# Optimization experiments

Hardware: AMD Instinct MI355X
Metric: run time of the kernel (lower is better)

## Reference

```python
import jax, jax.numpy as jnp
import numpy as np

# Config mirrors module init: C=12 channels, include_time=True -> d=13, depth=3
# sig_channels = d + d^2 + d^3 = 2379

def setup_inputs() -> dict:
    key = jax.random.key(0)
    k1, k2, k3 = jax.random.split(key, 3)
    N, C, J, T, L = 8, 12, 25, 64, 5
    d = C + 1
    sig_channels = d + d * d + d ** 3  # 2379
    out_dim = 256
    x = jax.random.normal(k1, (N, C, J, T, L), dtype=jnp.float32)
    W = jax.random.normal(k2, (out_dim, sig_channels), dtype=jnp.float32) / np.sqrt(sig_channels)
    b = jax.random.normal(k3, (out_dim,), dtype=jnp.float32) * 0.01
    return {"x": x, "W": W, "b": b}


def _signature_depth3(path):
    """Truncated (depth 3) path signature with zero basepoint.
    path: [B, L, d] -> sig: [B, d + d^2 + d^3]
    Chen's identity: s <- s * exp(dx), with exp(dx)_n = dx^{(x)n} / n!
    """
    B, L, d = path.shape
    # basepoint=True: prepend zeros, then take increments
    inc = jnp.diff(jnp.concatenate([jnp.zeros((B, 1, d), path.dtype), path], axis=1), axis=1)  # [B, L, d]

    def step(carry, dx):
        s1, s2, s3 = carry  # [B,d], [B,d*d], [B,d^3]
        e2 = 0.5 * jnp.einsum('bi,bj->bij', dx, dx)                     # [B,d,d]
        e3 = (jnp.einsum('bij,bk->bijk', e2, dx) / 3.0).reshape(B, d ** 3)  # dx^3/6
        n1 = s1 + dx
        n2 = s2 + jnp.einsum('bi,bj->bij', s1, dx).reshape(B, d * d) + e2.reshape(B, d * d)
        n3 = (s3
              + jnp.einsum('bij,bk->bijk', s2.reshape(B, d, d), dx).reshape(B, d ** 3)
              + jnp.einsum('bi,bjk->bijk', s1, e2).reshape(B, d ** 3)
              + e3)
        return (n1, n2, n3), None

    init = (jnp.zeros((B, d), path.dtype),
            jnp.zeros((B, d * d), path.dtype),
            jnp.zeros((B, d ** 3), path.dtype))
    (s1, s2, s3), _ = jax.lax.scan(step, init, jnp.moveaxis(inc, 1, 0))
    return jnp.concatenate([s1, s2, s3], axis=-1)


def reference(x, W, b):
    N, C, J, T, L = x.shape
    B = J * T * N
    # windowed gather: block (i*T+j)*N..(..+1)*N = x[:,:,i,j,:].permute(0,2,1)
    path = jnp.transpose(x, (2, 3, 0, 4, 1)).reshape(B, L, C)  # [J*T*N, L, C]
    # Augment include_time=True: append time channel linspace(0,1,L)
    t = jnp.linspace(0.0, 1.0, L, dtype=path.dtype)
    path = jnp.concatenate([path, jnp.broadcast_to(t[None, :, None], (B, L, 1))], axis=-1)
    sig = _signature_depth3(path)                 # [B, 2379]
    z = sig @ W.T + b                             # [B, out_dim]
    # scatter back: res[:, :, i, j] = z[(i*T+j)*N : ...]
    return jnp.transpose(z.reshape(J, T, N, -1), (2, 3, 0, 1))  # [N, out_dim, J, T]
```

## Files before the change

### kernel.cpp

```cpp
#include <hip/hip_runtime.h>
#include <hip/hip_bf16.h>

typedef float f32x4 __attribute__((ext_vector_type(4)));
typedef short s16x8 __attribute__((ext_vector_type(8)));

#define SIGC 2379
#define KPAD 2432
#define NKT  76
#define NKT_HALF 38
#define SROW 2440
#define NPATH 12800


__device__ inline void split2(float v, __hip_bfloat16* h, __hip_bfloat16* l) {
    __hip_bfloat16 hh = __float2bfloat16(v);
    *h = hh;
    *l = __float2bfloat16(v - __bfloat162float(hh));
}

__device__ inline void gload_lds16(const __hip_bfloat16* g, __hip_bfloat16* l) {
    __builtin_amdgcn_global_load_lds(
        (const __attribute__((address_space(1))) void*)g,
        (__attribute__((address_space(3))) void*)l,
        16, 0, 0);
}

__global__ __launch_bounds__(256) void wconv_kernel(const float* __restrict__ W,
                                                    __hip_bfloat16* __restrict__ Wh,
                                                    __hip_bfloat16* __restrict__ Wl)
{
    int k = blockIdx.x * 256 + threadIdx.x;
    int n = blockIdx.y;
    if (k >= KPAD) return;
    float v = (k < SIGC) ? W[(size_t)n * SIGC + k] : 0.0f;
    size_t off = ((size_t)(n >> 4) * NKT + (k >> 5)) * 512 + ((k >> 3) & 3) * 128 + (n & 15) * 8 + (k & 7);
    split2(v, &Wh[off], &Wl[off]);
}

__global__ __launch_bounds__(256) void sig_kernel(const float* __restrict__ x,
                                                  __hip_bfloat16* __restrict__ Ah,
                                                  __hip_bfloat16* __restrict__ Al_,
                                                  int r_start)
{
    __shared__ float inc_s[4][5][16];
    __shared__ __align__(16) __hip_bfloat16 hi_s[4][SROW];
    __shared__ __align__(16) __hip_bfloat16 lo_s[4][SROW];

    const int t = threadIdx.x;
    const int w = t >> 6;
    const int lane = t & 63;

    const int p0 = lane;
    const int p1 = lane + 64;
    const int p2 = lane + 128;
    const bool has2 = (p2 < 169);
    const int i0 = p0 / 13, j0 = p0 - i0 * 13;
    const int i1 = p1 / 13, j1 = p1 - i1 * 13;
    const int i2 = p2 / 13, j2 = p2 - i2 * 13;

    for (int pp = 0; pp < 4; ++pp) {
        const int r = r_start + blockIdx.x * 16 + pp * 4 + w;
        const int nn = r & 7;
        const int jj = (r >> 3) & 63;
        const int ii = r >> 9;

        __syncthreads();
        if (lane < 13) {
            if (lane < 12) {
                const float* px = x + ((size_t)(nn * 12 + lane) * 1600 + ii * 64 + jj) * 5;
                float prev = 0.0f;
                #pragma unroll
                for (int l = 0; l < 5; ++l) {
                    float v = px[l];
                    inc_s[w][l][lane] = v - prev;
                    prev = v;
                }
            } else {
                inc_s[w][0][12] = 0.0f;
                #pragma unroll
                for (int l = 1; l < 5; ++l) inc_s[w][l][12] = 0.25f;
            }
        }
        __syncthreads();

        float s1i0 = 0.0f, s1i1 = 0.0f, s1i2 = 0.0f;
        float s2p0 = 0.0f, s2p1 = 0.0f, s2p2 = 0.0f;
        float s1own = 0.0f;
        float s3a[13], s3b[13], s3c[13];
        #pragma unroll
        for (int k = 0; k < 13; ++k) { s3a[k] = 0.0f; s3b[k] = 0.0f; s3c[k] = 0.0f; }

        for (int l = 0; l < 5; ++l) {
            float dxl[13];
            #pragma unroll
            for (int k = 0; k < 13; ++k) dxl[k] = inc_s[w][l][k];

            {
                float dxi = inc_s[w][l][i0];
                float dxj = inc_s[w][l][j0];
                float C   = s2p0 + 0.5f * dxj * (s1i0 + dxi * (1.0f / 3.0f));
                #pragma unroll
                for (int k = 0; k < 13; ++k) s3a[k] += dxl[k] * C;
                s2p0 += s1i0 * dxj + 0.5f * dxi * dxj;
                s1i0 += dxi;
            }
            {
                float dxi = inc_s[w][l][i1];
                float dxj = inc_s[w][l][j1];
                float C   = s2p1 + 0.5f * dxj * (s1i1 + dxi * (1.0f / 3.0f));
                #pragma unroll
                for (int k = 0; k < 13; ++k) s3b[k] += dxl[k] * C;
                s2p1 += s1i1 * dxj + 0.5f * dxi * dxj;
                s1i1 += dxi;
            }
            if (has2) {
                float dxi = inc_s[w][l][i2];
                float dxj = inc_s[w][l][j2];
                float C   = s2p2 + 0.5f * dxj * (s1i2 + dxi * (1.0f / 3.0f));
                #pragma unroll
                for (int k = 0; k < 13; ++k) s3c[k] += dxl[k] * C;
                s2p2 += s1i2 * dxj + 0.5f * dxi * dxj;
                s1i2 += dxi;
            }
            if (lane < 13) s1own += inc_s[w][l][lane];
        }

        if (lane < 13) split2(s1own, &hi_s[w][lane], &lo_s[w][lane]);
        split2(s2p0, &hi_s[w][13 + p0], &lo_s[w][13 + p0]);
        split2(s2p1, &hi_s[w][13 + p1], &lo_s[w][13 + p1]);
        if (has2) split2(s2p2, &hi_s[w][13 + p2], &lo_s[w][13 + p2]);
        #pragma unroll
        for (int k = 0; k < 13; ++k) split2(s3a[k], &hi_s[w][182 + p0 * 13 + k], &lo_s[w][182 + p0 * 13 + k]);
        #pragma unroll
        for (int k = 0; k < 13; ++k) split2(s3b[k], &hi_s[w][182 + p1 * 13 + k], &lo_s[w][182 + p1 * 13 + k]);
        if (has2) {
            #pragma unroll
            for (int k = 0; k < 13; ++k) split2(s3c[k], &hi_s[w][182 + p2 * 13 + k], &lo_s[w][182 + p2 * 13 + k]);
        }
        if (lane < KPAD - SIGC) {
            hi_s[w][SIGC + lane] = __float2bfloat16(0.0f);
            lo_s[w][SIGC + lane] = __float2bfloat16(0.0f);
        }

        __syncthreads();

        const int rtl = blockIdx.x;
        const int rr = t & 3, ks = (t >> 2) & 3, ts = t >> 4;
        #pragma unroll
        for (int it2 = 0; it2 < 5; ++it2) {
            int kt = it2 * 16 + ts;
            if (kt < NKT) {
                size_t off = ((size_t)rtl * NKT + kt) * 512 + ks * 128 + (pp * 4 + rr) * 8;
                int lidx = kt * 32 + ks * 8;
                *reinterpret_cast<int4*>(Ah + off)  = *reinterpret_cast<const int4*>(&hi_s[rr][lidx]);
                *reinterpret_cast<int4*>(Al_ + off) = *reinterpret_cast<const int4*>(&lo_s[rr][lidx]);
            }
        }
    }
}

__global__ __launch_bounds__(256) void gemm_kernel(const __hip_bfloat16* __restrict__ Ah,
                                                   const __hip_bfloat16* __restrict__ Al_,
                                                   const __hip_bfloat16* __restrict__ Wh,
                                                   const __hip_bfloat16* __restrict__ Wl,
                                                   float* __restrict__ P,
                                                   int chunk_alloc, int nmblk)
{
    __shared__ __align__(16) __hip_bfloat16 L[3][32 * 512];

    const int bid = blockIdx.x;
    const int x8 = bid & 7;
    const int h = (bid >> 3) & 1;
    const int ksp = (bid >> 4) & 1;
    const int q = bid >> 5;
    const int mIdx = q * 8 + x8;
    if (mIdx >= nmblk) return;

    const int t = threadIdx.x;
    const int lane = t & 63;
    const int w = t >> 6;
    const int wm = w >> 1, wn = w & 1;
    const int rt0 = mIdx * 8;
    const int nt0 = h * 8;
    const int kt0 = ksp * NKT_HALF;

    f32x4 acc[4][4] = {};

    auto stage = [&](int buf, int kt) {
        #pragma unroll
        for (int s = 0; s < 8; ++s) {
            int tt = w * 8 + s;
            const __hip_bfloat16* g;
            if (tt < 8)       g = Ah  + ((size_t)(rt0 + tt)       * NKT + kt) * 512;
            else if (tt < 16) g = Al_ + ((size_t)(rt0 + tt - 8)   * NKT + kt) * 512;
            else if (tt < 24) g = Wh  + ((size_t)(nt0 + tt - 16)  * NKT + kt) * 512;
            else              g = Wl  + ((size_t)(nt0 + tt - 24)  * NKT + kt) * 512;
            gload_lds16(g + lane * 8, &L[buf][tt * 512]);
        }
    };

    auto compute = [&](int lb) {
        const __hip_bfloat16* Lb = &L[lb][0];
        s16x8 ah[4], al4[4], bh[4], bl4[4];
        #pragma unroll
        for (int mm = 0; mm < 4; ++mm) {
            ah[mm]  = *reinterpret_cast<const s16x8*>(&Lb[(wm * 4 + mm) * 512 + lane * 8]);
            al4[mm] = *reinterpret_cast<const s16x8*>(&Lb[(8 + wm * 4 + mm) * 512 + lane * 8]);
        }
        #pragma unroll
        for (int nn = 0; nn < 4; ++nn) {
            bh[nn]  = *reinterpret_cast<const s16x8*>(&Lb[(16 + wn * 4 + nn) * 512 + lane * 8]);
            bl4[nn] = *reinterpret_cast<const s16x8*>(&Lb[(24 + wn * 4 + nn) * 512 + lane * 8]);
        }
        __builtin_amdgcn_s_setprio(1);
        #pragma unroll
        for (int nn = 0; nn < 4; ++nn)
            #pragma unroll
            for (int mm = 0; mm < 4; ++mm) {
                acc[mm][nn] = __builtin_amdgcn_mfma_f32_16x16x32_bf16(ah[mm],  bh[nn],  acc[mm][nn], 0, 0, 0);
                acc[mm][nn] = __builtin_amdgcn_mfma_f32_16x16x32_bf16(ah[mm],  bl4[nn], acc[mm][nn], 0, 0, 0);
                acc[mm][nn] = __builtin_amdgcn_mfma_f32_16x16x32_bf16(al4[mm], bh[nn],  acc[mm][nn], 0, 0, 0);
            }
        __builtin_amdgcn_s_setprio(0);
    };

    stage(0, kt0);
    stage(1, kt0 + 1);

    #pragma unroll 1
    for (int kk = 0; kk < NKT_HALF; ++kk) {
        if (kk + 2 < NKT_HALF) stage((kk + 2) % 3, kt0 + kk + 2);
        if (kk + 2 < NKT_HALF)      asm volatile("s_waitcnt vmcnt(16)" ::: "memory");
        else if (kk + 1 < NKT_HALF) asm volatile("s_waitcnt vmcnt(8)" ::: "memory");
        else                        asm volatile("s_waitcnt vmcnt(0)" ::: "memory");
        __builtin_amdgcn_s_barrier();
        asm volatile("" ::: "memory");
        compute(kk % 3);
        asm volatile("" ::: "memory");
        __builtin_amdgcn_s_barrier();
    }

    float* Pb = P + ((size_t)ksp * chunk_alloc + mIdx * 128) * 256 + h * 128;
    #pragma unroll
    for (int mm = 0; mm < 4; ++mm)
        #pragma unroll
        for (int nn = 0; nn < 4; ++nn) {
            int o = wn * 64 + nn * 16 + (lane & 15);
            #pragma unroll
            for (int rr = 0; rr < 4; ++rr) {
                int p = wm * 64 + mm * 16 + (lane >> 4) * 4 + rr;
                Pb[(size_t)p * 256 + o] = acc[mm][nn][rr];
            }
        }
}

__global__ __launch_bounds__(256) void reduce_kernel(const float* __restrict__ P,
                                                     const float* __restrict__ b,
                                                     float* __restrict__ out,
                                                     int chunk_alloc, int r_start)
{
    const int mb = blockIdx.x;
    const int pbase = r_start + mb * 64;
    const int ii = pbase >> 9;
    const int jj0 = (pbase >> 3) & 63;
    const int t = threadIdx.x;
    const int ol = t >> 1, hh = t & 1;

    const float* P0 = P + (size_t)mb * 64 * 256;
    const size_t ps = (size_t)chunk_alloc * 256;

    int o = blockIdx.y * 128 + ol;
    float bo = b[o];
    #pragma unroll
    for (int c = 0; c < 4; ++c) {
        int ni = hh * 4 + c;
        float v[8];
        #pragma unroll
        for (int qq = 0; qq < 8; ++qq) {
            size_t idx = (size_t)(qq * 8 + ni) * 256 + o;
            v[qq] = P0[idx] + P0[idx + ps] + bo;
        }
        float* dst = out + (size_t)(ni * 256 + o) * 1600 + ii * 64 + jj0;
        *reinterpret_cast<float4*>(dst)     = make_float4(v[0], v[1], v[2], v[3]);
        *reinterpret_cast<float4*>(dst + 4) = make_float4(v[4], v[5], v[6], v[7]);
    }
}

extern "C" void kernel_launch(void* const* d_in, const int* in_sizes, int n_in,
                              void* d_out, int out_size, void* d_ws, size_t ws_size,
                              hipStream_t stream)
{
    const float* x = (const float*)d_in[0];
    const float* W = (const float*)d_in[1];
    const float* b = (const float*)d_in[2];
    float* out = (float*)d_out;

    char* ws = (char*)d_ws;
    __hip_bfloat16* Wh = (__hip_bfloat16*)ws;
    __hip_bfloat16* Wl = Wh + (size_t)16 * NKT * 512;
    size_t a_off = (((size_t)16 * NKT * 512 * 2 * 2) + 255) & ~(size_t)255;

    size_t avail = (ws_size > a_off) ? ws_size - a_off : 0;
    long long maxp = (long long)(avail / ((size_t)KPAD * 4 + 2048));
    int chunk = (int)((maxp / 128) * 128);
    if (chunk > NPATH) chunk = NPATH;
    if (chunk < 128) chunk = 128;

    __hip_bfloat16* Ah = (__hip_bfloat16*)(ws + a_off);
    __hip_bfloat16* Al_ = Ah + (size_t)chunk * KPAD;
    float* P = (float*)(Al_ + (size_t)chunk * KPAD);

    wconv_kernel<<<dim3(10, 256), 256, 0, stream>>>(W, Wh, Wl);

    for (int r0 = 0; r0 < NPATH; r0 += chunk) {
        int cnt = NPATH - r0;
        if (cnt > chunk) cnt = chunk;
        int nmblk = cnt / 128;
        int nblk = ((nmblk + 7) / 8) * 32;
        sig_kernel<<<dim3(cnt / 16), 256, 0, stream>>>(x, Ah, Al_, r0);
        gemm_kernel<<<dim3(nblk), 256, 0, stream>>>(Ah, Al_, Wh, Wl, P, chunk, nmblk);
        reduce_kernel<<<dim3(cnt / 64, 2), 256, 0, stream>>>(P, b, out, chunk, r0);
    }
}
```

Baseline: 125.8 us.

## Drop split-K in GEMM and fuse bias/transpose epilogue into GEMM kernel

The GEMM no longer splits K into two halves. Each block now runs the full 76 K-tiles, and the separate reduce kernel is removed. The accumulator tile is staged through LDS and written straight to the output with bias added and the permuted layout applied. This removes the fp32 partial-sum buffer round trip and one kernel launch, but halves the GEMM grid (fewer blocks, about 200 for 100 M-blocks) and doubles the serial K loop per block, which may underfill the 256 CUs.

```diff
diff --git a/kernel.cpp b/kernel.cpp
--- a/kernel.cpp
+++ b/kernel.cpp
@@ -7,7 +7,6 @@
 #define SIGC 2379
 #define KPAD 2432
 #define NKT  76
-#define NKT_HALF 38
 #define SROW 2440
 #define NPATH 12800
 
@@ -163,16 +162,16 @@
                                                    const __hip_bfloat16* __restrict__ Al_,
                                                    const __hip_bfloat16* __restrict__ Wh,
                                                    const __hip_bfloat16* __restrict__ Wl,
-                                                   float* __restrict__ P,
-                                                   int chunk_alloc, int nmblk)
+                                                   const float* __restrict__ b,
+                                                   float* __restrict__ out,
+                                                   int r_start, int nmblk)
 {
     __shared__ __align__(16) __hip_bfloat16 L[3][32 * 512];
 
     const int bid = blockIdx.x;
     const int x8 = bid & 7;
     const int h = (bid >> 3) & 1;
-    const int ksp = (bid >> 4) & 1;
-    const int q = bid >> 5;
+    const int q = bid >> 4;
     const int mIdx = q * 8 + x8;
     if (mIdx >= nmblk) return;
 
@@ -182,7 +181,6 @@
     const int wm = w >> 1, wn = w & 1;
     const int rt0 = mIdx * 8;
     const int nt0 = h * 8;
-    const int kt0 = ksp * NKT_HALF;
 
     f32x4 acc[4][4] = {};
 
@@ -224,65 +222,57 @@
         __builtin_amdgcn_s_setprio(0);
     };
 
-    stage(0, kt0);
-    stage(1, kt0 + 1);
+    stage(0, 0);
+    stage(1, 1);
+    int b0 = 0, b1 = 1, b2 = 2;
 
     #pragma unroll 1
-    for (int kk = 0; kk < NKT_HALF; ++kk) {
-        if (kk + 2 < NKT_HALF) stage((kk + 2) % 3, kt0 + kk + 2);
-        if (kk + 2 < NKT_HALF)      asm volatile("s_waitcnt vmcnt(16)" ::: "memory");
-        else if (kk + 1 < NKT_HALF) asm volatile("s_waitcnt vmcnt(8)" ::: "memory");
-        else                        asm volatile("s_waitcnt vmcnt(0)" ::: "memory");
+    for (int kt = 0; kt < NKT; ++kt) {
+        if (kt + 2 < NKT) {
+            stage(b2, kt + 2);
+            asm volatile("s_waitcnt vmcnt(16)" ::: "memory");
+        } else if (kt + 1 < NKT) {
+            asm volatile("s_waitcnt vmcnt(8)" ::: "memory");
+        } else {
+            asm volatile("s_waitcnt vmcnt(0)" ::: "memory");
+        }
         __builtin_amdgcn_s_barrier();
-        asm volatile("" ::: "memory");
-        compute(kk % 3);
-        asm volatile("" ::: "memory");
+        compute(b0);
         __builtin_amdgcn_s_barrier();
+        int tmp = b0; b0 = b1; b1 = b2; b2 = tmp;
     }
 
-    float* Pb = P + ((size_t)ksp * chunk_alloc + mIdx * 128) * 256 + h * 128;
+    __syncthreads();
+    float* T = (float*)&L[0][0];
     #pragma unroll
     for (int mm = 0; mm < 4; ++mm)
         #pragma unroll
-        for (int nn = 0; nn < 4; ++nn) {
-            int o = wn * 64 + nn * 16 + (lane & 15);
+        for (int nn = 0; nn < 4; ++nn)
             #pragma unroll
             for (int rr = 0; rr < 4; ++rr) {
                 int p = wm * 64 + mm * 16 + (lane >> 4) * 4 + rr;
-                Pb[(size_t)p * 256 + o] = acc[mm][nn][rr];
-            }
-        }
-}
-
-__global__ __launch_bounds__(256) void reduce_kernel(const float* __restrict__ P,
-                                                     const float* __restrict__ b,
-                                                     float* __restrict__ out,
-                                                     int chunk_alloc, int r_start)
-{
-    const int mb = blockIdx.x;
-    const int pbase = r_start + mb * 64;
+                int o = wn * 64 + nn * 16 + (lane & 15);
+                T[p * 132 + o] = acc[mm][nn][rr];
+            }
+    __syncthreads();
+
+    const int pbase = r_start + mIdx * 128;
     const int ii = pbase >> 9;
     const int jj0 = (pbase >> 3) & 63;
-    const int t = threadIdx.x;
     const int ol = t >> 1, hh = t & 1;
-
-    const float* P0 = P + (size_t)mb * 64 * 256;
-    const size_t ps = (size_t)chunk_alloc * 256;
-
-    int o = blockIdx.y * 128 + ol;
-    float bo = b[o];
+    const int o = h * 128 + ol;
+    const float bo = b[o];
     #pragma unroll
     for (int c = 0; c < 4; ++c) {
         int ni = hh * 4 + c;
-        float v[8];
-        #pragma unroll
-        for (int qq = 0; qq < 8; ++qq) {
-            size_t idx = (size_t)(qq * 8 + ni) * 256 + o;
-            v[qq] = P0[idx] + P0[idx + ps] + bo;
-        }
+        float v[16];
+        #pragma unroll
+        for (int qq = 0; qq < 16; ++qq) v[qq] = T[(qq * 8 + ni) * 132 + ol] + bo;
         float* dst = out + (size_t)(ni * 256 + o) * 1600 + ii * 64 + jj0;
-        *reinterpret_cast<float4*>(dst)     = make_float4(v[0], v[1], v[2], v[3]);
-        *reinterpret_cast<float4*>(dst + 4) = make_float4(v[4], v[5], v[6], v[7]);
+        *reinterpret_cast<float4*>(dst)      = make_float4(v[0],  v[1],  v[2],  v[3]);
+        *reinterpret_cast<float4*>(dst + 4)  = make_float4(v[4],  v[5],  v[6],  v[7]);
+        *reinterpret_cast<float4*>(dst + 8)  = make_float4(v[8],  v[9],  v[10], v[11]);
+        *reinterpret_cast<float4*>(dst + 12) = make_float4(v[12], v[13], v[14], v[15]);
     }
 }
 
@@ -301,14 +291,13 @@
     size_t a_off = (((size_t)16 * NKT * 512 * 2 * 2) + 255) & ~(size_t)255;
 
     size_t avail = (ws_size > a_off) ? ws_size - a_off : 0;
-    long long maxp = (long long)(avail / ((size_t)KPAD * 4 + 2048));
+    long long maxp = (long long)(avail / ((size_t)KPAD * 4));
     int chunk = (int)((maxp / 128) * 128);
     if (chunk > NPATH) chunk = NPATH;
     if (chunk < 128) chunk = 128;
 
     __hip_bfloat16* Ah = (__hip_bfloat16*)(ws + a_off);
     __hip_bfloat16* Al_ = Ah + (size_t)chunk * KPAD;
-    float* P = (float*)(Al_ + (size_t)chunk * KPAD);
 
     wconv_kernel<<<dim3(10, 256), 256, 0, stream>>>(W, Wh, Wl);
 
@@ -316,9 +305,8 @@
         int cnt = NPATH - r0;
         if (cnt > chunk) cnt = chunk;
         int nmblk = cnt / 128;
-        int nblk = ((nmblk + 7) / 8) * 32;
+        int nblk = ((nmblk + 7) / 8) * 16;
         sig_kernel<<<dim3(cnt / 16), 256, 0, stream>>>(x, Ah, Al_, r0);
-        gemm_kernel<<<dim3(nblk), 256, 0, stream>>>(Ah, Al_, Wh, Wl, P, chunk, nmblk);
-        reduce_kernel<<<dim3(cnt / 64, 2), 256, 0, stream>>>(P, b, out, chunk, r0);
+        gemm_kernel<<<dim3(nblk), 256, 0, stream>>>(Ah, Al_, Wh, Wl, b, out, r0, nmblk);
     }
 }
```

New measurement: 113.0 us. -10.2%, faster.
